# Performance work log

Hardware: AMD Instinct MI355X
Metric: run time of the kernel (lower is better)

## Reference

```python
import jax, jax.numpy as jnp
import numpy as np

B, T, C, H = 64, 256, 384, 6
HS = C // H  # 64


def _ln(x, w, b, eps=1e-5):
    m = jnp.mean(x, axis=-1, keepdims=True)
    v = jnp.mean((x - m) ** 2, axis=-1, keepdims=True)
    return (x - m) / jnp.sqrt(v + eps) * w + b


def setup_inputs() -> dict:
    key = jax.random.key(0)
    ks = jax.random.split(key, 18)
    sc = 0.02
    return {
        "x": jax.random.normal(ks[0], (B, T, C), jnp.float32),
        "ln1_w": jnp.ones((C,), jnp.float32),
        "ln1_b": jnp.zeros((C,), jnp.float32),
        # per-head Q/K/V linears stacked over the head axis: [H, C, HS]
        "Wq": jax.random.normal(ks[1], (H, C, HS), jnp.float32) * sc,
        "bq": jnp.zeros((H, HS), jnp.float32),
        "Wk": jax.random.normal(ks[2], (H, C, HS), jnp.float32) * sc,
        "bk": jnp.zeros((H, HS), jnp.float32),
        "Wv": jax.random.normal(ks[3], (H, C, HS), jnp.float32) * sc,
        "bv": jnp.zeros((H, HS), jnp.float32),
        "Wproj": jax.random.normal(ks[4], (C, C), jnp.float32) * sc,
        "bproj": jnp.zeros((C,), jnp.float32),
        "ln2_w": jnp.ones((C,), jnp.float32),
        "ln2_b": jnp.zeros((C,), jnp.float32),
        "W1": jax.random.normal(ks[5], (C, 4 * C), jnp.float32) * sc,
        "b1": jnp.zeros((4 * C,), jnp.float32),
        "W2": jax.random.normal(ks[6], (4 * C, C), jnp.float32) * sc,
        "b2": jnp.zeros((C,), jnp.float32),
    }


def reference(x, ln1_w, ln1_b, Wq, bq, Wk, bk, Wv, bv, Wproj, bproj,
              ln2_w, ln2_b, W1, b1, W2, b2):
    # --- pre-norm causal MHA (dropout = identity in eval) ---
    h = _ln(x, ln1_w, ln1_b)
    Q = jnp.einsum('btc,hcd->bhtd', h, Wq) + bq[None, :, None, :]
    K = jnp.einsum('btc,hcd->bhtd', h, Wk) + bk[None, :, None, :]
    V = jnp.einsum('btc,hcd->bhtd', h, Wv) + bv[None, :, None, :]
    scores = jnp.einsum('bhtd,bhsd->bhts', Q, K) * (HS ** -0.5)
    mask = jnp.tril(jnp.ones((x.shape[1], x.shape[1]), bool))
    scores = jnp.where(mask, scores, -jnp.inf)
    wei = jax.nn.softmax(scores, axis=-1)
    o = jnp.einsum('bhts,bhsd->bhtd', wei, V)
    # concat heads (same order as torch.cat over head list)
    o = o.transpose(0, 2, 1, 3).reshape(x.shape[0], x.shape[1], C)
    x1 = x + o @ Wproj + bproj
    # --- pre-norm FFN with exact (erf) GELU, matching torch default ---
    h2 = _ln(x1, ln2_w, ln2_b)
    f = jax.nn.gelu(h2 @ W1 + b1, approximate=False) @ W2 + b2
    return x1 + f
```

## Files before the change

kernel.cpp:

```cpp
#include <hip/hip_runtime.h>
#include <math.h>

constexpr int Bsz  = 64;
constexpr int Tseq = 256;
constexpr int Cdim = 384;
constexpr int Hh   = 6;
constexpr int HSd  = 64;
constexpr int Mrows = Bsz * Tseq;
constexpr int Cffn  = 4 * Cdim;
constexpr int Nqkv  = 3 * Cdim;

typedef __attribute__((ext_vector_type(8))) short short8;
typedef __attribute__((ext_vector_type(4))) float f32x4;

__device__ __forceinline__ ushort f2bf(float x) {
  union { float f; uint u; } a; a.f = x;
  uint r = a.u + 0x7fffu + ((a.u >> 16) & 1u);
  return (ushort)(r >> 16);
}
__device__ __forceinline__ float bf2f(ushort u) {
  union { uint u; float f; } a; a.u = ((uint)u) << 16;
  return a.f;
}
__device__ __forceinline__ uint pk_bf16(float lo, float hi) {
  uint r;
  asm("v_cvt_pk_bf16_f32 %0, %1, %2" : "=v"(r) : "v"(lo), "v"(hi));
  return r;
}

__device__ __forceinline__ float gelu_fast(float x) {
  float t = x * x;
  float u = x * fmaf(0.044715f, t, 1.0f);
  float e = fminf(1.5957691216f * u, 80.f);
  float z = __expf(e);
  return x * (z / (1.0f + z));
}

__global__ __launch_bounds__(256) void prep_kernel(
    const float* __restrict__ Wq, const float* __restrict__ Wk,
    const float* __restrict__ Wv, const float* __restrict__ Wproj,
    const float* __restrict__ W1, const float* __restrict__ W2,
    const float* __restrict__ bq, const float* __restrict__ bk,
    const float* __restrict__ bv,
    const float* __restrict__ x, const float* __restrict__ ln1_w,
    const float* __restrict__ ln1_b,
    ushort* __restrict__ WqkvT, ushort* __restrict__ WprojT,
    ushort* __restrict__ W1T, ushort* __restrict__ W2T,
    float* __restrict__ bqkv, ushort* __restrict__ hOut) {
  const int bid = blockIdx.x;
  if (bid >= 1733) {
    const int row  = (bid - 1733) * 4 + (threadIdx.x >> 6);
    const int lane = threadIdx.x & 63;
    if (row >= Mrows) return;
    const float* xr = x + (size_t)row * Cdim;
    float v[6];
    float s = 0.f;
#pragma unroll
    for (int i = 0; i < 6; ++i) { v[i] = xr[lane + 64 * i]; s += v[i]; }
#pragma unroll
    for (int off = 32; off > 0; off >>= 1) s += __shfl_xor(s, off, 64);
    float mean = s * (1.f / Cdim);
    float sq = 0.f;
#pragma unroll
    for (int i = 0; i < 6; ++i) { float d = v[i] - mean; sq += d * d; }
#pragma unroll
    for (int off = 32; off > 0; off >>= 1) sq += __shfl_xor(sq, off, 64);
    float rstd = rsqrtf(sq * (1.f / Cdim) + 1e-5f);
    ushort* orow = hOut + (size_t)row * Cdim;
#pragma unroll
    for (int i = 0; i < 6; ++i) {
      int c = lane + 64 * i;
      orow[c] = f2bf((v[i] - mean) * rstd * ln1_w[c] + ln1_b[c]);
    }
    return;
  }
  if (bid >= 1728) {
    int i = (bid - 1728) * 256 + threadIdx.x;
    if (i < Nqkv)
      bqkv[i] = (i < 384) ? bq[i] : (i < 768) ? bk[i - 384] : bv[i - 768];
    return;
  }
  const int tx = threadIdx.x & 31, ty = threadIdx.x >> 5;
  const float* src; ushort* dst; int R, S, r0, s0, perm = 0;
  if (bid < 432) {
    int which = bid / 144, rem = bid % 144;
    const float* W = (which == 0) ? Wq : (which == 1) ? Wk : Wv;
    int bz = rem / 24, t = rem % 24;
    R = 384; S = 64;
    src = W + (size_t)bz * R * S;
    dst = WqkvT + (size_t)which * 384 * 384 + (size_t)bz * R * S;
    r0 = (t >> 1) * 32; s0 = (t & 1) * 32;
  } else if (bid < 576) {
    int rem = bid - 432; R = 384; S = 384; src = Wproj; dst = WprojT;
    r0 = (rem / 12) * 32; s0 = (rem % 12) * 32; perm = 1;
  } else if (bid < 1152) {
    int rem = bid - 576; R = 384; S = 1536; src = W1; dst = W1T;
    r0 = (rem / 48) * 32; s0 = (rem % 48) * 32;
  } else {
    int rem = bid - 1152; R = 1536; S = 384; src = W2; dst = W2T;
    r0 = (rem / 12) * 32; s0 = (rem % 12) * 32; perm = 1;
  }
  __shared__ float t[32][33];
#pragma unroll
  for (int i = 0; i < 32; i += 8)
    t[ty + i][tx] = src[(size_t)(r0 + ty + i) * S + s0 + tx];
  __syncthreads();
  const int kk = r0 + tx;
  int kp = kk;
  if (perm) kp = (kk & ~63) | (((kk & 15) << 2) | ((kk >> 4) & 3));
#pragma unroll
  for (int i = 0; i < 32; i += 8)
    dst[(size_t)(s0 + ty + i) * R + kp] = f2bf(t[tx][ty + i]);
}

template <typename T>
__global__ __launch_bounds__(256) void ln_kernel(
    const T* __restrict__ x, const float* __restrict__ w,
    const float* __restrict__ b, ushort* __restrict__ out, int nrows) {
  int row  = blockIdx.x * 4 + (threadIdx.x >> 6);
  int lane = threadIdx.x & 63;
  if (row >= nrows) return;
  const T* xr = x + (size_t)row * Cdim;
  float v[6];
  float s = 0.f;
#pragma unroll
  for (int i = 0; i < 6; ++i) {
    if constexpr (sizeof(T) == 2) v[i] = bf2f(xr[lane + 64 * i]);
    else                          v[i] = xr[lane + 64 * i];
    s += v[i];
  }
#pragma unroll
  for (int off = 32; off > 0; off >>= 1) s += __shfl_xor(s, off, 64);
  float mean = s * (1.f / Cdim);
  float sq = 0.f;
#pragma unroll
  for (int i = 0; i < 6; ++i) { float d = v[i] - mean; sq += d * d; }
#pragma unroll
  for (int off = 32; off > 0; off >>= 1) sq += __shfl_xor(sq, off, 64);
  float rstd = rsqrtf(sq * (1.f / Cdim) + 1e-5f);
  ushort* orow = out + (size_t)row * Cdim;
#pragma unroll
  for (int i = 0; i < 6; ++i) {
    int c = lane + 64 * i;
    orow[c] = f2bf((v[i] - mean) * rstd * w[c] + b[c]);
  }
}

template <int EPI, int BN, int NN, int KK>
__global__ __launch_bounds__(512) void mfma_gemm(
    const ushort* __restrict__ A, const ushort* __restrict__ Bt,
    const float* __restrict__ bias, const void* __restrict__ res,
    void* __restrict__ Cout, void* __restrict__ C2, void* __restrict__ C3) {
  constexpr int WC  = BN / 2;
  constexpr int JN  = WC / 16;
  constexpr int NBQ = BN / 64;
  constexpr int nt  = KK >> 6;
  __shared__ ushort Als[2 * 128 * 64];
  __shared__ ushort Bls[2 * BN * 64];
  const int tid = threadIdx.x;

  const int lid = blockIdx.y * gridDim.x + blockIdx.x;
  const int xcd = lid & 7, idx = lid >> 3;
  const int by = xcd * 16 + (idx & 15);
  const int bx = idx >> 4;
  const int m0 = by * 128, n0 = bx * BN;

  const int lane = tid & 63;
  const int w    = tid >> 6;
  const int wr   = (w & 3) * 32;
  const int wc   = (w >> 2) * WC;
  const int lm   = lane & 15;
  const int g    = lane >> 4;
  const int rq   = g * 4;

  const int wub = (tid & ~63) * 8;

  f32x4 acc[2][JN] = {};

  const ushort* gA0;
  const ushort* gA1;
  const ushort* gB0;
  const ushort* gB1;
  {
    const int ciA0 = tid, ciA1 = tid + 512;
    gA0 = A + (size_t)(m0 + (ciA0 >> 3)) * KK + ((ciA0 & 7) ^ ((ciA0 >> 3) & 7)) * 8;
    gA1 = A + (size_t)(m0 + (ciA1 >> 3)) * KK + ((ciA1 & 7) ^ ((ciA1 >> 3) & 7)) * 8;
    const int ciB0 = tid, ciB1 = tid + 512;
    gB0 = Bt + (size_t)(n0 + (ciB0 >> 3)) * KK + ((ciB0 & 7) ^ ((ciB0 >> 3) & 7)) * 8;
    gB1 = (NBQ == 2)
        ? Bt + (size_t)(n0 + (ciB1 >> 3)) * KK + ((ciB1 & 7) ^ ((ciB1 >> 3) & 7)) * 8
        : gB0;
  }

  auto stage = [&](int bf) {
    ushort* Ab = Als + bf * (128 * 64);
    ushort* Bb = Bls + bf * (BN * 64);
    __builtin_amdgcn_global_load_lds(
        (const __attribute__((address_space(1))) uint*)gA0,
        (__attribute__((address_space(3))) uint*)(Ab + wub), 16, 0, 0);
    __builtin_amdgcn_global_load_lds(
        (const __attribute__((address_space(1))) uint*)gA1,
        (__attribute__((address_space(3))) uint*)(Ab + wub + 4096), 16, 0, 0);
    __builtin_amdgcn_global_load_lds(
        (const __attribute__((address_space(1))) uint*)gB0,
        (__attribute__((address_space(3))) uint*)(Bb + wub), 16, 0, 0);
    if (NBQ == 2)
      __builtin_amdgcn_global_load_lds(
          (const __attribute__((address_space(1))) uint*)gB1,
          (__attribute__((address_space(3))) uint*)(Bb + wub + 4096), 16, 0, 0);
    gA0 += 64; gA1 += 64; gB0 += 64;
    if (NBQ == 2) gB1 += 64;
  };

  stage(0);

  for (int t = 0; t < nt; ++t) {
    const int cur = t & 1;
    if (t + 1 < nt) {
      stage(cur ^ 1);
      if constexpr (NBQ == 2)
        asm volatile("s_waitcnt vmcnt(4)" ::: "memory");
      else
        asm volatile("s_waitcnt vmcnt(3)" ::: "memory");
    } else {
      asm volatile("s_waitcnt vmcnt(0)" ::: "memory");
    }
    __builtin_amdgcn_sched_barrier(0);
    __builtin_amdgcn_s_barrier();
    __builtin_amdgcn_sched_barrier(0);

    const ushort* Ab = Als + cur * (128 * 64);
    const ushort* Bb = Bls + cur * (BN * 64);
#pragma unroll
    for (int half = 0; half < 2; ++half) {
      const int sl = ((half << 2) | g) ^ (lm & 7);
      short8 af[2], bfr[JN];
#pragma unroll
      for (int i = 0; i < 2; ++i)
        af[i] = *(const short8*)&Ab[(wr + i * 16 + lm) * 64 + sl * 8];
#pragma unroll
      for (int j = 0; j < JN; ++j)
        bfr[j] = *(const short8*)&Bb[(wc + j * 16 + lm) * 64 + sl * 8];
      __builtin_amdgcn_s_setprio(1);
#pragma unroll
      for (int i = 0; i < 2; ++i)
#pragma unroll
        for (int j = 0; j < JN; ++j)
          acc[i][j] = __builtin_amdgcn_mfma_f32_16x16x32_bf16(af[i], bfr[j],
                                                              acc[i][j], 0, 0, 0);
      __builtin_amdgcn_s_setprio(0);
    }

    asm volatile("s_waitcnt lgkmcnt(0)" ::: "memory");
    __builtin_amdgcn_sched_barrier(0);
    __builtin_amdgcn_s_barrier();
    __builtin_amdgcn_sched_barrier(0);
  }

  float bb[JN];
#pragma unroll
  for (int j = 0; j < JN; ++j) bb[j] = bias[n0 + wc + j * 16 + lm];

#pragma unroll
  for (int i = 0; i < 2; ++i) {
#pragma unroll
    for (int r = 0; r < 4; ++r) {
      const int row = m0 + wr + i * 16 + rq + r;
      if constexpr (EPI == 1) {
        const float* resrow = (const float*)res + (size_t)row * NN + n0 + wc;
        ushort* crow = (ushort*)Cout + (size_t)row * NN + n0 + wc;
#pragma unroll
        for (int j = 0; j < JN; ++j) {
          float rv = __builtin_nontemporal_load(resrow + j * 16 + lm);
          crow[j * 16 + lm] = f2bf(acc[i][j][r] + bb[j] + rv);
        }
      } else if constexpr (EPI == 4) {
        const ushort* resrow = (const ushort*)res + (size_t)row * NN + n0 + wc;
        float* crow = (float*)Cout + (size_t)row * NN + n0 + wc;
#pragma unroll
        for (int j = 0; j < JN; ++j)
          crow[j * 16 + lm] = acc[i][j][r] + bb[j] + bf2f(resrow[j * 16 + lm]);
      } else if constexpr (EPI == 3) {
        ushort* crow = (ushort*)Cout + (size_t)row * NN + n0 + wc + lm * 4;
        uint d0 = pk_bf16(acc[i][0][r] + bb[0], acc[i][1][r] + bb[1]);
        uint d1 = pk_bf16(acc[i][2][r] + bb[2], acc[i][3][r] + bb[3]);
        uint2 pkv; pkv.x = d0; pkv.y = d1;
        *(uint2*)crow = pkv;
      } else {
        ushort* crow = (ushort*)Cout + (size_t)row * NN + n0 + wc + lm * 4;
        float g0 = gelu_fast(acc[i][0][r] + bb[0]);
        float g1 = gelu_fast(acc[i][1][r] + bb[1]);
        float g2 = gelu_fast(acc[i][2][r] + bb[2]);
        float g3 = gelu_fast(acc[i][3][r] + bb[3]);
        uint d0 = pk_bf16(g0, g1);
        uint d1 = pk_bf16(g2, g3);
        uint2 pkv; pkv.x = d0; pkv.y = d1;
        *(uint2*)crow = pkv;
      }
    }
  }
}

__global__ __launch_bounds__(256) void attn_kernel(
    const ushort* __restrict__ QKV, ushort* __restrict__ Oc) {
  __shared__ ushort Ks[64 * 72];
  __shared__ ushort Vt[64 * 72];
  __shared__ ushort Pl[4][16 * 72];
  const int bh = blockIdx.x, qt = blockIdx.y;
  const int b = bh / Hh, h = bh % Hh;
  const int tid = threadIdx.x;
  const int w = tid >> 6, lane = tid & 63;
  const int g = lane >> 4, n16 = lane & 15;

  const ushort* qrow =
      QKV + (size_t)(b * Tseq + qt * 64 + w * 16 + n16) * Nqkv + h * HSd;
  short8 qf0 = *(const short8*)(qrow + g * 8);
  short8 qf1 = *(const short8*)(qrow + 32 + g * 8);

  f32x4 oacc[4] = {};
  float m_r[4], l_r[4];
#pragma unroll
  for (int r = 0; r < 4; ++r) { m_r[r] = -1e30f; l_r[r] = 0.f; }

  const int t0 = qt * 64 + w * 16 + g * 4;

  const ushort* Ksrc = QKV + (size_t)b * Tseq * Nqkv + Cdim + h * HSd;
  const ushort* Vsrc = QKV + (size_t)b * Tseq * Nqkv + 2 * Cdim + h * HSd;

  for (int st = 0; st <= qt; ++st) {
    __syncthreads();
    for (int c = tid; c < 512; c += 256) {
      int kr = c >> 3, kc = (c & 7) * 8;
      *(uint4*)&Ks[kr * 72 + kc] =
          *(const uint4*)&Ksrc[(size_t)(st * 64 + kr) * Nqkv + kc];
      int vr = c & 63, vc = (c >> 6) * 8;
      uint4 vv = *(const uint4*)&Vsrc[(size_t)(st * 64 + vr) * Nqkv + vc];
      const ushort* pv = (const ushort*)&vv;
#pragma unroll
      for (int i = 0; i < 8; ++i) Vt[(vc + i) * 72 + vr] = pv[i];
    }
    __syncthreads();

    f32x4 s[4];
#pragma unroll
    for (int ct = 0; ct < 4; ++ct) {
      short8 kf0 = *(const short8*)&Ks[(ct * 16 + n16) * 72 + g * 8];
      short8 kf1 = *(const short8*)&Ks[(ct * 16 + n16) * 72 + 32 + g * 8];
      f32x4 z = {};
      z = __builtin_amdgcn_mfma_f32_16x16x32_bf16(qf0, kf0, z, 0, 0, 0);
      z = __builtin_amdgcn_mfma_f32_16x16x32_bf16(qf1, kf1, z, 0, 0, 0);
      s[ct] = z;
    }

#pragma unroll
    for (int ct = 0; ct < 4; ++ct) {
      const int s_col = st * 64 + ct * 16 + n16;
#pragma unroll
      for (int r = 0; r < 4; ++r) {
        float v = s[ct][r] * 0.125f;
        s[ct][r] = (s_col > t0 + r) ? -1e30f : v;
      }
    }

#pragma unroll
    for (int r = 0; r < 4; ++r) {
      float m = fmaxf(fmaxf(s[0][r], s[1][r]), fmaxf(s[2][r], s[3][r]));
      m = fmaxf(m, __shfl_xor(m, 1, 64));
      m = fmaxf(m, __shfl_xor(m, 2, 64));
      m = fmaxf(m, __shfl_xor(m, 4, 64));
      m = fmaxf(m, __shfl_xor(m, 8, 64));
      float mnew = fmaxf(m_r[r], m);
      float alpha = __expf(m_r[r] - mnew);
      m_r[r] = mnew;
      float ssum = 0.f;
#pragma unroll
      for (int ct = 0; ct < 4; ++ct) {
        float p = __expf(s[ct][r] - mnew);
        s[ct][r] = p;
        ssum += p;
      }
      ssum += __shfl_xor(ssum, 1, 64);
      ssum += __shfl_xor(ssum, 2, 64);
      ssum += __shfl_xor(ssum, 4, 64);
      ssum += __shfl_xor(ssum, 8, 64);
      l_r[r] = l_r[r] * alpha + ssum;
#pragma unroll
      for (int j = 0; j < 4; ++j) oacc[j][r] *= alpha;
    }

    ushort* pw = &Pl[w][0];
#pragma unroll
    for (int ct = 0; ct < 4; ++ct)
#pragma unroll
      for (int r = 0; r < 4; ++r)
        pw[(g * 4 + r) * 72 + ct * 16 + n16] = f2bf(s[ct][r]);

    short8 pf0 = *(const short8*)&pw[n16 * 72 + g * 8];
    short8 pf1 = *(const short8*)&pw[n16 * 72 + 32 + g * 8];
#pragma unroll
    for (int j = 0; j < 4; ++j) {
      short8 vf0 = *(const short8*)&Vt[(j * 16 + n16) * 72 + g * 8];
      short8 vf1 = *(const short8*)&Vt[(j * 16 + n16) * 72 + 32 + g * 8];
      oacc[j] = __builtin_amdgcn_mfma_f32_16x16x32_bf16(pf0, vf0, oacc[j], 0, 0, 0);
      oacc[j] = __builtin_amdgcn_mfma_f32_16x16x32_bf16(pf1, vf1, oacc[j], 0, 0, 0);
    }
  }

  float inv[4];
#pragma unroll
  for (int r = 0; r < 4; ++r) inv[r] = 1.f / l_r[r];
  ushort* orow = Oc + ((size_t)(b * Tseq + qt * 64 + w * 16)) * Cdim + h * HSd;
#pragma unroll
  for (int j = 0; j < 4; ++j)
#pragma unroll
    for (int r = 0; r < 4; ++r)
      orow[(size_t)(g * 4 + r) * Cdim + j * 16 + n16] = f2bf(oacc[j][r] * inv[r]);
}

extern "C" void kernel_launch(void* const* d_in, const int* in_sizes, int n_in,
                              void* d_out, int out_size, void* d_ws, size_t ws_size,
                              hipStream_t stream) {
  const float* x      = (const float*)d_in[0];
  const float* ln1_w  = (const float*)d_in[1];
  const float* ln1_b  = (const float*)d_in[2];
  const float* Wq     = (const float*)d_in[3];
  const float* bq     = (const float*)d_in[4];
  const float* Wk     = (const float*)d_in[5];
  const float* bk     = (const float*)d_in[6];
  const float* Wv     = (const float*)d_in[7];
  const float* bv     = (const float*)d_in[8];
  const float* Wproj  = (const float*)d_in[9];
  const float* bproj  = (const float*)d_in[10];
  const float* ln2_w  = (const float*)d_in[11];
  const float* ln2_b  = (const float*)d_in[12];
  const float* W1     = (const float*)d_in[13];
  const float* b1     = (const float*)d_in[14];
  const float* W2     = (const float*)d_in[15];
  const float* b2     = (const float*)d_in[16];
  float* out = (float*)d_out;

  char* p = (char*)d_ws;
  ushort* h     = (ushort*)p;  p += (size_t)Mrows * Cdim * 2;
  ushort* QKV   = (ushort*)p;  p += (size_t)Mrows * Nqkv * 2;
  ushort* Oc    = (ushort*)p;  p += (size_t)Mrows * Cdim * 2;
  ushort* g     = (ushort*)p;  p += (size_t)Mrows * Cffn * 2;
  ushort* WqkvT = (ushort*)p;  p += (size_t)Nqkv * Cdim * 2;
  ushort* WprojT= (ushort*)p;  p += (size_t)Cdim * Cdim * 2;
  ushort* W1T   = (ushort*)p;  p += (size_t)Cffn * Cdim * 2;
  ushort* W2T   = (ushort*)p;  p += (size_t)Cdim * Cffn * 2;
  float*  bqkv  = (float*)p;   p += (size_t)Nqkv * 4;
  ushort* h2 = h;
  ushort* x1 = QKV;

  dim3 blk(256), blk512(512);

  prep_kernel<<<dim3(1733 + Mrows / 4), blk, 0, stream>>>(
      Wq, Wk, Wv, Wproj, W1, W2, bq, bk, bv, x, ln1_w, ln1_b,
      WqkvT, WprojT, W1T, W2T, bqkv, h);

  mfma_gemm<3, 128, Nqkv, Cdim><<<dim3(Nqkv / 128, Mrows / 128), blk512, 0, stream>>>(
      h, WqkvT, bqkv, nullptr, QKV, nullptr, nullptr);

  attn_kernel<<<dim3(Bsz * Hh, 4), blk, 0, stream>>>(QKV, Oc);

  mfma_gemm<1, 64, Cdim, Cdim><<<dim3(Cdim / 64, Mrows / 128), blk512, 0, stream>>>(
      Oc, WprojT, bproj, x, x1, nullptr, nullptr);

  ln_kernel<ushort><<<dim3(Mrows / 4), blk, 0, stream>>>(x1, ln2_w, ln2_b, h2, Mrows);

  mfma_gemm<2, 128, Cffn, Cdim><<<dim3(Cffn / 128, Mrows / 128), blk512, 0, stream>>>(
      h2, W1T, b1, nullptr, g, nullptr, nullptr);

  mfma_gemm<4, 64, Cdim, Cffn><<<dim3(Cdim / 64, Mrows / 128), blk512, 0, stream>>>(
      g, W2T, b2, x1, out, nullptr, nullptr);
}
```

Measured before the change: 233.2 us.

## Prefetch next K/V tile into registers and raise MFMA wave priority

The attention kernel now loads the next K/V tile from global memory into registers before computing on the current tile, and writes it to shared memory after the compute and a barrier. This overlaps global load latency with the QK and PV MFMA work. It also wraps the MFMA calls in s_setprio to favour matrix issue. The cost is extra registers per thread, which could lower occupancy.

```diff
diff --git a/kernel.cpp b/kernel.cpp
--- a/kernel.cpp
+++ b/kernel.cpp
@@ -327,18 +327,34 @@
   const ushort* Ksrc = QKV + (size_t)b * Tseq * Nqkv + Cdim + h * HSd;
   const ushort* Vsrc = QKV + (size_t)b * Tseq * Nqkv + 2 * Cdim + h * HSd;
 
+  const int kr0 = tid >> 3, kc0 = (tid & 7) * 8;
+  const int kr1 = kr0 + 32;
+  const int vr  = tid & 63;
+  const int vc0 = (tid >> 6) * 8, vc1 = vc0 + 32;
+
+  uint4 k0v, k1v, v0v, v1v;
+  auto load_tile = [&](int st) {
+    k0v = *(const uint4*)&Ksrc[(size_t)(st * 64 + kr0) * Nqkv + kc0];
+    k1v = *(const uint4*)&Ksrc[(size_t)(st * 64 + kr1) * Nqkv + kc0];
+    v0v = *(const uint4*)&Vsrc[(size_t)(st * 64 + vr) * Nqkv + vc0];
+    v1v = *(const uint4*)&Vsrc[(size_t)(st * 64 + vr) * Nqkv + vc1];
+  };
+  auto write_tile = [&]() {
+    *(uint4*)&Ks[kr0 * 72 + kc0] = k0v;
+    *(uint4*)&Ks[kr1 * 72 + kc0] = k1v;
+    const ushort* p0 = (const ushort*)&v0v;
+#pragma unroll
+    for (int i = 0; i < 8; ++i) Vt[(vc0 + i) * 72 + vr] = p0[i];
+    const ushort* p1 = (const ushort*)&v1v;
+#pragma unroll
+    for (int i = 0; i < 8; ++i) Vt[(vc1 + i) * 72 + vr] = p1[i];
+  };
+
+  load_tile(0);
+  write_tile();
+
   for (int st = 0; st <= qt; ++st) {
-    __syncthreads();
-    for (int c = tid; c < 512; c += 256) {
-      int kr = c >> 3, kc = (c & 7) * 8;
-      *(uint4*)&Ks[kr * 72 + kc] =
-          *(const uint4*)&Ksrc[(size_t)(st * 64 + kr) * Nqkv + kc];
-      int vr = c & 63, vc = (c >> 6) * 8;
-      uint4 vv = *(const uint4*)&Vsrc[(size_t)(st * 64 + vr) * Nqkv + vc];
-      const ushort* pv = (const ushort*)&vv;
-#pragma unroll
-      for (int i = 0; i < 8; ++i) Vt[(vc + i) * 72 + vr] = pv[i];
-    }
+    if (st < qt) load_tile(st + 1);
     __syncthreads();
 
     f32x4 s[4];
@@ -347,8 +363,10 @@
       short8 kf0 = *(const short8*)&Ks[(ct * 16 + n16) * 72 + g * 8];
       short8 kf1 = *(const short8*)&Ks[(ct * 16 + n16) * 72 + 32 + g * 8];
       f32x4 z = {};
+      __builtin_amdgcn_s_setprio(1);
       z = __builtin_amdgcn_mfma_f32_16x16x32_bf16(qf0, kf0, z, 0, 0, 0);
       z = __builtin_amdgcn_mfma_f32_16x16x32_bf16(qf1, kf1, z, 0, 0, 0);
+      __builtin_amdgcn_s_setprio(0);
       s[ct] = z;
     }
 
@@ -401,9 +419,14 @@
     for (int j = 0; j < 4; ++j) {
       short8 vf0 = *(const short8*)&Vt[(j * 16 + n16) * 72 + g * 8];
       short8 vf1 = *(const short8*)&Vt[(j * 16 + n16) * 72 + 32 + g * 8];
+      __builtin_amdgcn_s_setprio(1);
       oacc[j] = __builtin_amdgcn_mfma_f32_16x16x32_bf16(pf0, vf0, oacc[j], 0, 0, 0);
       oacc[j] = __builtin_amdgcn_mfma_f32_16x16x32_bf16(pf1, vf1, oacc[j], 0, 0, 0);
-    }
+      __builtin_amdgcn_s_setprio(0);
+    }
+
+    __syncthreads();
+    if (st < qt) write_tile();
   }
 
   float inv[4];
```

Measured after the change: 230.3 us. About the same (-1.2%).
